# Kernel optimization log

Hardware: AMD Instinct MI355X
Metric: run time of the kernel (lower is better)

The kernel has to match this reference:

```python
import jax, jax.numpy as jnp
import numpy as np

N_NODES = 50000
N_EDGES = 800000
IN_DIM = 128
OUT_DIM = 128
NUM_RELS = 8


def setup_inputs() -> dict:
    key = jax.random.key(0)
    k_feat, k_rel, k_w, k_src, k_dst, k_rt = jax.random.split(key, 6)
    feat = jax.random.normal(k_feat, (N_NODES, IN_DIM), dtype=jnp.float32)
    # xavier_uniform over (in_dim, out_dim) fan
    limit = float(np.sqrt(6.0 / (IN_DIM + OUT_DIM)))
    rel_emb = jax.random.uniform(k_rel, (NUM_RELS, IN_DIM, OUT_DIM), dtype=jnp.float32,
                                 minval=-limit, maxval=limit)
    edge_weight = jax.random.uniform(k_w, (N_EDGES,), dtype=jnp.float32)
    src = jax.random.randint(k_src, (N_EDGES,), 0, N_NODES, dtype=jnp.int32)
    dst = jax.random.randint(k_dst, (N_EDGES,), 0, N_NODES, dtype=jnp.int32)
    rel_type = jax.random.randint(k_rt, (N_EDGES,), 0, NUM_RELS, dtype=jnp.int32)
    return {"feat": feat, "rel_emb": rel_emb, "edge_weight": edge_weight,
            "src": src, "dst": dst, "rel_type": rel_type}


def reference(feat, rel_emb, edge_weight, src, dst, rel_type):
    # src_feat: [E, in] gather of source-node features
    src_feat = feat[src]
    num_rels = rel_emb.shape[0]
    # Equivalent to bmm(src_feat[:,None,:], rel_emb[rel_type]).squeeze(1)
    # but avoids materializing the [E, in, out] per-edge weight tensor:
    # loop over the small fixed relation set with masked accumulation.
    msg = jnp.zeros((src_feat.shape[0], rel_emb.shape[2]), dtype=src_feat.dtype)
    for r in range(num_rels):
        mask = (rel_type == r)[:, None]
        msg = msg + jnp.where(mask, src_feat @ rel_emb[r], jnp.zeros((), dtype=src_feat.dtype))
    msg = msg * edge_weight[:, None]
    # copy_e + sum aggregation onto destination nodes: [N, out]
    return jax.ops.segment_sum(msg, dst, num_segments=feat.shape[0])
```

## Files before the change

### kernel.cpp

```cpp
#include <hip/hip_runtime.h>
#include <stdint.h>

#define N_NODES   50000
#define N_EDGES   800000
#define IN_DIM    128
#define OUT_DIM   128
#define NUM_RELS  8
#define THREADS   256

typedef _Float16 half_t;
typedef _Float16 half2v __attribute__((ext_vector_type(2)));
typedef _Float16 half4v __attribute__((ext_vector_type(4)));
typedef _Float16 half8 __attribute__((ext_vector_type(8)));
typedef float floatx4 __attribute__((ext_vector_type(4)));


#define NBINS3    N_NODES
#define NB3       ((NBINS3 + 1023) / 1024)

#define WS_Y2     0
#define WS_OFF    102400000
#define WS_WT     102600064
#define WS_BASE   102862208
#define WS_WGT    106062208
#define WS_HIST   107662208
#define WS_BSUM   107862208
#define WS_NEED   (size_t)107862464

#define HIST_BLOCKS ((N_EDGES + 511) / 512)
__global__ void prep_hist_kernel(const float* __restrict__ rel_emb, half_t* __restrict__ WT,
                                 const int* __restrict__ dst, int* __restrict__ hist) {
    int b = blockIdx.x;
    if (b < 512) {
        int t = b * 256 + threadIdx.x;
        int r = t >> 14, k = (t >> 7) & 127, n = t & 127;
        WT[(size_t)((r << 7) | n) * 128 + k] = (half_t)rel_emb[t];
    } else {
        int i = (b - 512) * 512 + threadIdx.x;
        int d0 = (i < N_EDGES) ? dst[i] : -1;
        int d1 = (i + 256 < N_EDGES) ? dst[i + 256] : -1;
        if (d0 >= 0) atomicAdd(&hist[d0], 1);
        if (d1 >= 0) atomicAdd(&hist[d1], 1);
    }
}

__global__ void scan1_kernel(const int* __restrict__ hist, int* __restrict__ bsum) {
    __shared__ int sh[256];
    int b = blockIdx.x, t = threadIdx.x;
    int i0 = b * 1024 + t * 4;
    int s = 0;
    #pragma unroll
    for (int j = 0; j < 4; j++) { int idx = i0 + j; if (idx < NBINS3) s += hist[idx]; }
    sh[t] = s; __syncthreads();
    for (int o = 128; o > 0; o >>= 1) { if (t < o) sh[t] += sh[t + o]; __syncthreads(); }
    if (t == 0) bsum[b] = sh[0];
}

__global__ void scan2_kernel(int* __restrict__ bsum, int* __restrict__ off) {
    __shared__ int sh[64];
    int t = threadIdx.x;
    int v = (t < NB3) ? bsum[t] : 0;
    sh[t] = v; __syncthreads();
    for (int o = 1; o < 64; o <<= 1) {
        int x = (t >= o) ? sh[t - o] : 0;
        __syncthreads();
        sh[t] += x;
        __syncthreads();
    }
    if (t < NB3) bsum[t] = sh[t] - v;
    if (t == 0) off[NBINS3] = N_EDGES;
}

__global__ void scan3_kernel(const int* __restrict__ hist, const int* __restrict__ boff,
                             int* __restrict__ off, int* __restrict__ cursors) {
    __shared__ int sh[256];
    int b = blockIdx.x, t = threadIdx.x;
    int i0 = b * 1024 + t * 4;
    int v[4]; int s = 0;
    #pragma unroll
    for (int j = 0; j < 4; j++) { int idx = i0 + j; v[j] = (idx < NBINS3) ? hist[idx] : 0; s += v[j]; }
    sh[t] = s; __syncthreads();
    for (int o = 1; o < 256; o <<= 1) {
        int x = (t >= o) ? sh[t - o] : 0;
        __syncthreads();
        sh[t] += x;
        __syncthreads();
    }
    int run = sh[t] - s + boff[b];
    #pragma unroll
    for (int j = 0; j < 4; j++) {
        int idx = i0 + j;
        if (idx < NBINS3) { off[idx] = run; cursors[idx] = run; }
        run += v[j];
    }
}

template<bool GUARD>
__device__ __forceinline__ void gemm_body(const float* __restrict__ feat,
                                          half_t* __restrict__ Ws,
                                          half_t* __restrict__ y2,
                                          int m0, int n0, int wave, int lane) {
    const int q = lane >> 4, l16 = lane & 15;
    const int wm0 = m0 + wave * 32;

    float4 fr[2][4][2];
    #pragma unroll
    for (int ms = 0; ms < 2; ms++) {
        int node = wm0 + ms * 16 + l16;
        const float* fb = feat + (size_t)node * 128 + q * 8;
        bool ok = !GUARD || node < N_NODES;
        #pragma unroll
        for (int kk = 0; kk < 4; kk++)
            #pragma unroll
            for (int h = 0; h < 2; h++) {
                float4 v = {0.f, 0.f, 0.f, 0.f};
                if (ok) v = *(const float4*)(fb + kk * 32 + h * 4);
                fr[ms][kk][h] = v;
            }
    }
    __syncthreads();

    half8 bf[2][4];
    #pragma unroll
    for (int ms = 0; ms < 2; ms++)
        #pragma unroll
        for (int kk = 0; kk < 4; kk++) {
            half8 hb;
            hb[0] = (half_t)fr[ms][kk][0].x; hb[1] = (half_t)fr[ms][kk][0].y;
            hb[2] = (half_t)fr[ms][kk][0].z; hb[3] = (half_t)fr[ms][kk][0].w;
            hb[4] = (half_t)fr[ms][kk][1].x; hb[5] = (half_t)fr[ms][kk][1].y;
            hb[6] = (half_t)fr[ms][kk][1].z; hb[7] = (half_t)fr[ms][kk][1].w;
            bf[ms][kk] = hb;
        }

    floatx4 acc[8][2];
    #pragma unroll
    for (int nt = 0; nt < 8; nt++)
        #pragma unroll
        for (int ms = 0; ms < 2; ms++) acc[nt][ms] = (floatx4){0.f, 0.f, 0.f, 0.f};

    #pragma unroll
    for (int kk = 0; kk < 4; kk++) {
        #pragma unroll
        for (int nt = 0; nt < 8; nt++) {
            int row = nt * 16 + l16;
            int phys = (kk * 4 + q) ^ (l16 & 7);
            half8 a = *(const half8*)(Ws + row * 128 + phys * 8);
            acc[nt][0] = __builtin_amdgcn_mfma_f32_16x16x32_f16(a, bf[0][kk], acc[nt][0], 0, 0, 0);
            acc[nt][1] = __builtin_amdgcn_mfma_f32_16x16x32_f16(a, bf[1][kk], acc[nt][1], 0, 0, 0);
        }
    }

    __syncthreads();
    #pragma unroll
    for (int nt = 0; nt < 8; nt++)
        #pragma unroll
        for (int ms = 0; ms < 2; ms++) {
            int nl = wave * 32 + ms * 16 + l16;
            int c  = nt * 4 + q;
            int p  = (c + nl) & 31;
            half4v hv;
            hv[0] = (half_t)acc[nt][ms][0]; hv[1] = (half_t)acc[nt][ms][1];
            hv[2] = (half_t)acc[nt][ms][2]; hv[3] = (half_t)acc[nt][ms][3];
            *(half4v*)(Ws + nl * 128 + p * 4) = hv;
        }
    #pragma unroll
    for (int i = 0; i < 8; i++) {
        int nl  = wave * 32 + i * 4 + (lane >> 4);
        int c16 = lane & 15;
        int p0 = (2 * c16 + nl) & 31;
        int p1 = (2 * c16 + 1 + nl) & 31;
        uint2 lo = *(const uint2*)(Ws + nl * 128 + p0 * 4);
        uint2 hi = *(const uint2*)(Ws + nl * 128 + p1 * 4);
        int node = m0 + nl;
        if (!GUARD || node < N_NODES) {
            uint4 v; v.x = lo.x; v.y = lo.y; v.z = hi.x; v.w = hi.y;
            *(uint4*)(y2 + (size_t)node * 1024 + n0 + c16 * 8) = v;
        }
    }
}

#define FUSE_BLOCKS 6256
__global__ __launch_bounds__(THREADS) void fused_kernel(
    const float* __restrict__ feat, const half_t* __restrict__ WT,
    half_t* __restrict__ y2,
    const int* __restrict__ dst, const int* __restrict__ src,
    const int* __restrict__ rel, const float* __restrict__ ew,
    int* __restrict__ cursors, int* __restrict__ base, half_t* __restrict__ wgt) {
    __shared__ half_t Ws[128 * 128];
    const int bid = blockIdx.x;
    const int t = threadIdx.x;

    if (((bid >> 3) & 1) == 0) {
        int work = (bid & 7) * 391 + (bid >> 4);
        int mt = work >> 3, nt8 = work & 7;
        const int m0 = mt * 128, n0 = nt8 * 128;
        const int wave = t >> 6, lane = t & 63;

        for (int i = t; i < 2048; i += THREADS) {
            int row = i >> 4, lc = i & 15;
            int phys = lc ^ (row & 7);
            *(uint4*)&Ws[row * 128 + phys * 8] =
                *(const uint4*)(WT + (size_t)(n0 + row) * 128 + lc * 8);
        }
        if (m0 + 128 <= N_NODES)
            gemm_body<false>(feat, Ws, y2, m0, n0, wave, lane);
        else
            gemm_body<true>(feat, Ws, y2, m0, n0, wave, lane);
    } else {
        int sblock = (bid >> 4) * 8 + (bid & 7);
        if (sblock >= 3125) return;
        int i = sblock * 256 + t;
        int pos = atomicAdd(&cursors[dst[i]], 1);
        base[pos] = src[i] * 1024 + rel[i] * 128;
        wgt[pos] = (half_t)ew[i];
    }
}

__global__ __launch_bounds__(THREADS) void gather_kernel(
    const half_t* __restrict__ y2, const int* __restrict__ base,
    const half_t* __restrict__ wgt, const int* __restrict__ off,
    float* __restrict__ out) {
    int g = blockIdx.x * 4 + (threadIdx.x >> 6);
    int lane = threadIdx.x & 63;
    int beg = off[g], end = off[g + 1];
    const half_t* yb = y2 + lane * 2;
    float ax = 0.f, ay = 0.f, cx = 0.f, cy = 0.f;
    int e = beg;
    for (; e + 8 <= end; e += 8) {
        int b0 = base[e], b1 = base[e + 1], b2 = base[e + 2], b3 = base[e + 3];
        int b4 = base[e + 4], b5 = base[e + 5], b6 = base[e + 6], b7 = base[e + 7];
        half2v v0 = *(const half2v*)(yb + b0);
        half2v v1 = *(const half2v*)(yb + b1);
        half2v v2 = *(const half2v*)(yb + b2);
        half2v v3 = *(const half2v*)(yb + b3);
        half2v v4 = *(const half2v*)(yb + b4);
        half2v v5 = *(const half2v*)(yb + b5);
        half2v v6 = *(const half2v*)(yb + b6);
        half2v v7 = *(const half2v*)(yb + b7);
        float w0 = (float)wgt[e],     w1 = (float)wgt[e + 1];
        float w2 = (float)wgt[e + 2], w3 = (float)wgt[e + 3];
        float w4 = (float)wgt[e + 4], w5 = (float)wgt[e + 5];
        float w6 = (float)wgt[e + 6], w7 = (float)wgt[e + 7];
        ax += w0 * (float)v0[0] + w1 * (float)v1[0];
        ay += w0 * (float)v0[1] + w1 * (float)v1[1];
        cx += w2 * (float)v2[0] + w3 * (float)v3[0];
        cy += w2 * (float)v2[1] + w3 * (float)v3[1];
        ax += w4 * (float)v4[0] + w5 * (float)v5[0];
        ay += w4 * (float)v4[1] + w5 * (float)v5[1];
        cx += w6 * (float)v6[0] + w7 * (float)v7[0];
        cy += w6 * (float)v6[1] + w7 * (float)v7[1];
    }
    for (; e + 2 <= end; e += 2) {
        int b0 = base[e], b1 = base[e + 1];
        float w0 = (float)wgt[e], w1 = (float)wgt[e + 1];
        half2v v0 = *(const half2v*)(yb + b0);
        half2v v1 = *(const half2v*)(yb + b1);
        ax += w0 * (float)v0[0] + w1 * (float)v1[0];
        ay += w0 * (float)v0[1] + w1 * (float)v1[1];
    }
    if (e < end) {
        int b0 = base[e];
        float w0 = (float)wgt[e];
        half2v v0 = *(const half2v*)(yb + b0);
        cx += w0 * (float)v0[0];
        cy += w0 * (float)v0[1];
    }
    float2 o; o.x = ax + cx; o.y = ay + cy;
    *(float2*)(out + (size_t)g * 128 + lane * 2) = o;
}

__global__ void naive_kernel(const float* __restrict__ feat, const float* __restrict__ rel_emb,
                             const float* __restrict__ ew, const int* __restrict__ src,
                             const int* __restrict__ dst, const int* __restrict__ rel,
                             float* __restrict__ out) {
    int wave = (blockIdx.x * blockDim.x + threadIdx.x) >> 6;
    int lane = threadIdx.x & 63;
    if (wave >= N_EDGES) return;
    const float* f = feat + (size_t)src[wave] * IN_DIM;
    const float* W = rel_emb + (size_t)rel[wave] * IN_DIM * OUT_DIM;
    float w = ew[wave];
    float a0 = 0.f, a1 = 0.f;
    for (int k = 0; k < IN_DIM; k++) {
        float fv = f[k];
        a0 += fv * W[k * OUT_DIM + lane];
        a1 += fv * W[k * OUT_DIM + 64 + lane];
    }
    int d = dst[wave];
    atomicAdd(&out[(size_t)d * OUT_DIM + lane], a0 * w);
    atomicAdd(&out[(size_t)d * OUT_DIM + 64 + lane], a1 * w);
}

extern "C" void kernel_launch(void* const* d_in, const int* in_sizes, int n_in,
                              void* d_out, int out_size, void* d_ws, size_t ws_size,
                              hipStream_t stream) {
    const float* feat    = (const float*)d_in[0];
    const float* rel_emb = (const float*)d_in[1];
    const float* ew      = (const float*)d_in[2];
    const int*   src     = (const int*)d_in[3];
    const int*   dst     = (const int*)d_in[4];
    const int*   rel     = (const int*)d_in[5];
    float* out = (float*)d_out;

    if (ws_size >= WS_NEED) {
        char* ws = (char*)d_ws;
        half_t* y2    = (half_t*)(ws + WS_Y2);
        int*    off   = (int*)(ws + WS_OFF);
        half_t* WT    = (half_t*)(ws + WS_WT);
        int*    basep = (int*)(ws + WS_BASE);
        half_t* wgt   = (half_t*)(ws + WS_WGT);
        int*    hist  = (int*)(ws + WS_HIST);
        int*    bsum  = (int*)(ws + WS_BSUM);

        hipMemsetAsync(hist, 0, (size_t)NBINS3 * 4, stream);
        prep_hist_kernel<<<512 + HIST_BLOCKS, THREADS, 0, stream>>>(rel_emb, WT, dst, hist);
        scan1_kernel<<<NB3, 256, 0, stream>>>(hist, bsum);
        scan2_kernel<<<1, 64, 0, stream>>>(bsum, off);
        scan3_kernel<<<NB3, 256, 0, stream>>>(hist, bsum, off, hist);
        fused_kernel<<<FUSE_BLOCKS, THREADS, 0, stream>>>(feat, WT, y2, dst, src, rel, ew,
                                                          hist, basep, wgt);
        gather_kernel<<<N_NODES / 4, THREADS, 0, stream>>>(y2, basep, wgt, off, out);
    } else {
        hipMemsetAsync(d_out, 0, (size_t)out_size * sizeof(float), stream);
        const long long total = (long long)N_EDGES * 64;
        const int blocks = (int)((total + THREADS - 1) / THREADS);
        naive_kernel<<<blocks, THREADS, 0, stream>>>(feat, rel_emb, ew, src, dst, rel, out);
    }
}
```

Measured before the change: 260.7 us.

## Widen gather loads to 16B per lane and batch histogram/scatter edges per thread

The gather kernel now splits each wave into four 16-lane groups. Each group handles a different edge and loads 16-byte half8 vectors instead of 4-byte half2. Partial sums are combined with cross-group shuffles before one lane group writes the output row. The histogram and scatter phases each process four edges per thread with the loads hoisted ahead of the atomics, which increases memory-level parallelism. The cost is more registers, a shuffle reduction per node, and partial-group waste when a node has few edges.

```diff
diff --git a/kernel.cpp b/kernel.cpp
--- a/kernel.cpp
+++ b/kernel.cpp
@@ -27,7 +27,7 @@
 #define WS_BSUM   107862208
 #define WS_NEED   (size_t)107862464
 
-#define HIST_BLOCKS ((N_EDGES + 511) / 512)
+#define HIST_BLOCKS ((N_EDGES + 1023) / 1024)
 __global__ void prep_hist_kernel(const float* __restrict__ rel_emb, half_t* __restrict__ WT,
                                  const int* __restrict__ dst, int* __restrict__ hist) {
     int b = blockIdx.x;
@@ -36,11 +36,16 @@
         int r = t >> 14, k = (t >> 7) & 127, n = t & 127;
         WT[(size_t)((r << 7) | n) * 128 + k] = (half_t)rel_emb[t];
     } else {
-        int i = (b - 512) * 512 + threadIdx.x;
-        int d0 = (i < N_EDGES) ? dst[i] : -1;
-        int d1 = (i + 256 < N_EDGES) ? dst[i + 256] : -1;
-        if (d0 >= 0) atomicAdd(&hist[d0], 1);
-        if (d1 >= 0) atomicAdd(&hist[d1], 1);
+        int i0 = (b - 512) * 1024 + threadIdx.x;
+        int d[4];
+        #pragma unroll
+        for (int j = 0; j < 4; j++) {
+            int i = i0 + j * 256;
+            d[j] = (i < N_EDGES) ? dst[i] : -1;
+        }
+        #pragma unroll
+        for (int j = 0; j < 4; j++)
+            if (d[j] >= 0) atomicAdd(&hist[d[j]], 1);
     }
 }
 
@@ -209,11 +214,24 @@
             gemm_body<true>(feat, Ws, y2, m0, n0, wave, lane);
     } else {
         int sblock = (bid >> 4) * 8 + (bid & 7);
-        if (sblock >= 3125) return;
-        int i = sblock * 256 + t;
-        int pos = atomicAdd(&cursors[dst[i]], 1);
-        base[pos] = src[i] * 1024 + rel[i] * 128;
-        wgt[pos] = (half_t)ew[i];
+        if (sblock >= HIST_BLOCKS) return;
+        int i0 = sblock * 1024 + t;
+        int d[4], s[4], r[4]; float w[4];
+        #pragma unroll
+        for (int j = 0; j < 4; j++) {
+            int i = i0 + j * 256;
+            d[j] = (i < N_EDGES) ? dst[i] : -1;
+            s[j] = 0; r[j] = 0; w[j] = 0.f;
+            if (d[j] >= 0) { s[j] = src[i]; r[j] = rel[i]; w[j] = ew[i]; }
+        }
+        #pragma unroll
+        for (int j = 0; j < 4; j++) {
+            if (d[j] >= 0) {
+                int pos = atomicAdd(&cursors[d[j]], 1);
+                base[pos] = s[j] * 1024 + r[j] * 128;
+                wgt[pos] = (half_t)w[j];
+            }
+        }
     }
 }
 
@@ -223,51 +241,47 @@
     float* __restrict__ out) {
     int g = blockIdx.x * 4 + (threadIdx.x >> 6);
     int lane = threadIdx.x & 63;
+    int q = lane >> 4, l16 = lane & 15;
     int beg = off[g], end = off[g + 1];
-    const half_t* yb = y2 + lane * 2;
-    float ax = 0.f, ay = 0.f, cx = 0.f, cy = 0.f;
+    const half_t* yb = y2 + l16 * 8;
+    float a0[8], a1[8];
+    #pragma unroll
+    for (int j = 0; j < 8; j++) { a0[j] = 0.f; a1[j] = 0.f; }
     int e = beg;
     for (; e + 8 <= end; e += 8) {
-        int b0 = base[e], b1 = base[e + 1], b2 = base[e + 2], b3 = base[e + 3];
-        int b4 = base[e + 4], b5 = base[e + 5], b6 = base[e + 6], b7 = base[e + 7];
-        half2v v0 = *(const half2v*)(yb + b0);
-        half2v v1 = *(const half2v*)(yb + b1);
-        half2v v2 = *(const half2v*)(yb + b2);
-        half2v v3 = *(const half2v*)(yb + b3);
-        half2v v4 = *(const half2v*)(yb + b4);
-        half2v v5 = *(const half2v*)(yb + b5);
-        half2v v6 = *(const half2v*)(yb + b6);
-        half2v v7 = *(const half2v*)(yb + b7);
-        float w0 = (float)wgt[e],     w1 = (float)wgt[e + 1];
-        float w2 = (float)wgt[e + 2], w3 = (float)wgt[e + 3];
-        float w4 = (float)wgt[e + 4], w5 = (float)wgt[e + 5];
-        float w6 = (float)wgt[e + 6], w7 = (float)wgt[e + 7];
-        ax += w0 * (float)v0[0] + w1 * (float)v1[0];
-        ay += w0 * (float)v0[1] + w1 * (float)v1[1];
-        cx += w2 * (float)v2[0] + w3 * (float)v3[0];
-        cy += w2 * (float)v2[1] + w3 * (float)v3[1];
-        ax += w4 * (float)v4[0] + w5 * (float)v5[0];
-        ay += w4 * (float)v4[1] + w5 * (float)v5[1];
-        cx += w6 * (float)v6[0] + w7 * (float)v7[0];
-        cy += w6 * (float)v6[1] + w7 * (float)v7[1];
-    }
-    for (; e + 2 <= end; e += 2) {
-        int b0 = base[e], b1 = base[e + 1];
-        float w0 = (float)wgt[e], w1 = (float)wgt[e + 1];
-        half2v v0 = *(const half2v*)(yb + b0);
-        half2v v1 = *(const half2v*)(yb + b1);
-        ax += w0 * (float)v0[0] + w1 * (float)v1[0];
-        ay += w0 * (float)v0[1] + w1 * (float)v1[1];
-    }
-    if (e < end) {
-        int b0 = base[e];
-        float w0 = (float)wgt[e];
-        half2v v0 = *(const half2v*)(yb + b0);
-        cx += w0 * (float)v0[0];
-        cy += w0 * (float)v0[1];
-    }
-    float2 o; o.x = ax + cx; o.y = ay + cy;
-    *(float2*)(out + (size_t)g * 128 + lane * 2) = o;
+        int e0 = e + q, e1 = e + 4 + q;
+        int b0 = base[e0], b1 = base[e1];
+        float w0 = (float)wgt[e0], w1 = (float)wgt[e1];
+        half8 v0 = *(const half8*)(yb + b0);
+        half8 v1 = *(const half8*)(yb + b1);
+        #pragma unroll
+        for (int j = 0; j < 8; j++) a0[j] += w0 * (float)v0[j];
+        #pragma unroll
+        for (int j = 0; j < 8; j++) a1[j] += w1 * (float)v1[j];
+    }
+    for (; e < end; e += 4) {
+        int ee = e + q;
+        int b0 = 0; float w0 = 0.f;
+        if (ee < end) { b0 = base[ee]; w0 = (float)wgt[ee]; }
+        half8 v0 = *(const half8*)(yb + b0);
+        #pragma unroll
+        for (int j = 0; j < 8; j++) a0[j] += w0 * (float)v0[j];
+    }
+    #pragma unroll
+    for (int j = 0; j < 8; j++) {
+        float s = a0[j] + a1[j];
+        s += __shfl_xor(s, 16);
+        s += __shfl_xor(s, 32);
+        a0[j] = s;
+    }
+    if (q == 0) {
+        float4 o0, o1;
+        o0.x = a0[0]; o0.y = a0[1]; o0.z = a0[2]; o0.w = a0[3];
+        o1.x = a0[4]; o1.y = a0[5]; o1.z = a0[6]; o1.w = a0[7];
+        float* ob = out + (size_t)g * 128 + l16 * 8;
+        *(float4*)ob = o0;
+        *(float4*)(ob + 4) = o1;
+    }
 }
 
 __global__ void naive_kernel(const float* __restrict__ feat, const float* __restrict__ rel_emb,
```

Result: no change. 257.6 us (-1.2%).

## Aggregate source features per relation before GEMM, using linked-list edge buckets

Applied to the files above, without the earlier changes.

The pipeline now aggregates weighted source features per destination node and per relation first, then runs one GEMM with K=1024 against the stacked relation weights, instead of transforming every node for all relations and gathering afterwards. The histogram plus three scan kernels are replaced by an atomicExch linked list built from dst. Launches drop from six kernels to three, and the y2 scatter buffer is replaced by an fp16 h buffer of the same size. The cost is a serial pointer-chasing walk per node with dependent loads, a per-edge branch on relation type, and edge order within each node that depends on atomic ordering.

```diff
diff --git a/kernel.cpp b/kernel.cpp
--- a/kernel.cpp
+++ b/kernel.cpp
@@ -10,264 +10,143 @@
 
 typedef _Float16 half_t;
 typedef _Float16 half2v __attribute__((ext_vector_type(2)));
-typedef _Float16 half4v __attribute__((ext_vector_type(4)));
 typedef _Float16 half8 __attribute__((ext_vector_type(8)));
 typedef float floatx4 __attribute__((ext_vector_type(4)));
 
 
-#define NBINS3    N_NODES
-#define NB3       ((NBINS3 + 1023) / 1024)
-
-#define WS_Y2     0
-#define WS_OFF    102400000
-#define WS_WT     102600064
-#define WS_BASE   102862208
-#define WS_WGT    106062208
-#define WS_HIST   107662208
-#define WS_BSUM   107862208
-#define WS_NEED   (size_t)107862464
-
-#define HIST_BLOCKS ((N_EDGES + 511) / 512)
-__global__ void prep_hist_kernel(const float* __restrict__ rel_emb, half_t* __restrict__ WT,
-                                 const int* __restrict__ dst, int* __restrict__ hist) {
+#define WS_H      0
+#define WS_WFT    102400000
+#define WS_HEAD   102662144
+#define WS_NEXT   102862144
+#define WS_NEED3  (size_t)106062144
+
+#define LIST_BLOCKS (N_EDGES / 256)
+
+__global__ void prep_kernel(const float* __restrict__ rel_emb, half_t* __restrict__ WfT,
+                            const int* __restrict__ dst, int* __restrict__ head,
+                            int* __restrict__ next) {
     int b = blockIdx.x;
     if (b < 512) {
         int t = b * 256 + threadIdx.x;
         int r = t >> 14, k = (t >> 7) & 127, n = t & 127;
-        WT[(size_t)((r << 7) | n) * 128 + k] = (half_t)rel_emb[t];
+        WfT[(size_t)n * 1024 + r * 128 + k] = (half_t)rel_emb[t];
     } else {
-        int i = (b - 512) * 512 + threadIdx.x;
-        int d0 = (i < N_EDGES) ? dst[i] : -1;
-        int d1 = (i + 256 < N_EDGES) ? dst[i + 256] : -1;
-        if (d0 >= 0) atomicAdd(&hist[d0], 1);
-        if (d1 >= 0) atomicAdd(&hist[d1], 1);
-    }
-}
-
-__global__ void scan1_kernel(const int* __restrict__ hist, int* __restrict__ bsum) {
-    __shared__ int sh[256];
-    int b = blockIdx.x, t = threadIdx.x;
-    int i0 = b * 1024 + t * 4;
-    int s = 0;
+        int i = (b - 512) * 256 + threadIdx.x;
+        next[i] = atomicExch(&head[dst[i]], i);
+    }
+}
+
+__global__ __launch_bounds__(THREADS) void agg_kernel(
+    const float* __restrict__ feat, const float* __restrict__ ew,
+    const int* __restrict__ src, const int* __restrict__ rel,
+    const int* __restrict__ head, const int* __restrict__ next,
+    half_t* __restrict__ h) {
+    int g = blockIdx.x * 4 + (threadIdx.x >> 6);
+    int lane = threadIdx.x & 63;
+
+    float a0x = 0.f, a0y = 0.f, a1x = 0.f, a1y = 0.f;
+    float a2x = 0.f, a2y = 0.f, a3x = 0.f, a3y = 0.f;
+    float a4x = 0.f, a4y = 0.f, a5x = 0.f, a5y = 0.f;
+    float a6x = 0.f, a6y = 0.f, a7x = 0.f, a7y = 0.f;
+
+    int e = head[g];
+    while (e >= 0) {
+        int nx  = next[e];
+        int sr  = src[e];
+        int re  = rel[e];
+        float w = ew[e];
+        float2 f = *(const float2*)(feat + (size_t)sr * 128 + lane * 2);
+        float wx = w * f.x, wy = w * f.y;
+        switch (re) {
+            case 0: a0x += wx; a0y += wy; break;
+            case 1: a1x += wx; a1y += wy; break;
+            case 2: a2x += wx; a2y += wy; break;
+            case 3: a3x += wx; a3y += wy; break;
+            case 4: a4x += wx; a4y += wy; break;
+            case 5: a5x += wx; a5y += wy; break;
+            case 6: a6x += wx; a6y += wy; break;
+            default: a7x += wx; a7y += wy; break;
+        }
+        e = nx;
+    }
+
+    half_t* hb = h + (size_t)g * 1024 + lane * 2;
+    *(half2v*)(hb + 0 * 128) = (half2v){(half_t)a0x, (half_t)a0y};
+    *(half2v*)(hb + 1 * 128) = (half2v){(half_t)a1x, (half_t)a1y};
+    *(half2v*)(hb + 2 * 128) = (half2v){(half_t)a2x, (half_t)a2y};
+    *(half2v*)(hb + 3 * 128) = (half2v){(half_t)a3x, (half_t)a3y};
+    *(half2v*)(hb + 4 * 128) = (half2v){(half_t)a4x, (half_t)a4y};
+    *(half2v*)(hb + 5 * 128) = (half2v){(half_t)a5x, (half_t)a5y};
+    *(half2v*)(hb + 6 * 128) = (half2v){(half_t)a6x, (half_t)a6y};
+    *(half2v*)(hb + 7 * 128) = (half2v){(half_t)a7x, (half_t)a7y};
+}
+
+template<bool GUARD>
+__device__ __forceinline__ void gemm2_body(const half_t* __restrict__ h,
+                                           const half_t* __restrict__ WfT,
+                                           half_t* __restrict__ Ws,
+                                           float* __restrict__ out,
+                                           int m0, int wave, int lane, int t) {
+    const int q = lane >> 4, l16 = lane & 15;
+    const int d = m0 + wave * 16 + l16;
+    const bool ok = !GUARD || d < N_NODES;
+    const half_t* hb = h + (size_t)d * 1024;
+
+    floatx4 acc[8];
     #pragma unroll
-    for (int j = 0; j < 4; j++) { int idx = i0 + j; if (idx < NBINS3) s += hist[idx]; }
-    sh[t] = s; __syncthreads();
-    for (int o = 128; o > 0; o >>= 1) { if (t < o) sh[t] += sh[t + o]; __syncthreads(); }
-    if (t == 0) bsum[b] = sh[0];
-}
-
-__global__ void scan2_kernel(int* __restrict__ bsum, int* __restrict__ off) {
-    __shared__ int sh[64];
-    int t = threadIdx.x;
-    int v = (t < NB3) ? bsum[t] : 0;
-    sh[t] = v; __syncthreads();
-    for (int o = 1; o < 64; o <<= 1) {
-        int x = (t >= o) ? sh[t - o] : 0;
-        __syncthreads();
-        sh[t] += x;
-        __syncthreads();
-    }
-    if (t < NB3) bsum[t] = sh[t] - v;
-    if (t == 0) off[NBINS3] = N_EDGES;
-}
-
-__global__ void scan3_kernel(const int* __restrict__ hist, const int* __restrict__ boff,
-                             int* __restrict__ off, int* __restrict__ cursors) {
-    __shared__ int sh[256];
-    int b = blockIdx.x, t = threadIdx.x;
-    int i0 = b * 1024 + t * 4;
-    int v[4]; int s = 0;
+    for (int nt = 0; nt < 8; nt++) acc[nt] = (floatx4){0.f, 0.f, 0.f, 0.f};
+
     #pragma unroll
-    for (int j = 0; j < 4; j++) { int idx = i0 + j; v[j] = (idx < NBINS3) ? hist[idx] : 0; s += v[j]; }
-    sh[t] = s; __syncthreads();
-    for (int o = 1; o < 256; o <<= 1) {
-        int x = (t >= o) ? sh[t - o] : 0;
-        __syncthreads();
-        sh[t] += x;
-        __syncthreads();
-    }
-    int run = sh[t] - s + boff[b];
-    #pragma unroll
-    for (int j = 0; j < 4; j++) {
-        int idx = i0 + j;
-        if (idx < NBINS3) { off[idx] = run; cursors[idx] = run; }
-        run += v[j];
-    }
-}
-
-template<bool GUARD>
-__device__ __forceinline__ void gemm_body(const float* __restrict__ feat,
-                                          half_t* __restrict__ Ws,
-                                          half_t* __restrict__ y2,
-                                          int m0, int n0, int wave, int lane) {
-    const int q = lane >> 4, l16 = lane & 15;
-    const int wm0 = m0 + wave * 32;
-
-    float4 fr[2][4][2];
-    #pragma unroll
-    for (int ms = 0; ms < 2; ms++) {
-        int node = wm0 + ms * 16 + l16;
-        const float* fb = feat + (size_t)node * 128 + q * 8;
-        bool ok = !GUARD || node < N_NODES;
-        #pragma unroll
-        for (int kk = 0; kk < 4; kk++)
-            #pragma unroll
-            for (int h = 0; h < 2; h++) {
-                float4 v = {0.f, 0.f, 0.f, 0.f};
-                if (ok) v = *(const float4*)(fb + kk * 32 + h * 4);
-                fr[ms][kk][h] = v;
-            }
-    }
-    __syncthreads();
-
-    half8 bf[2][4];
-    #pragma unroll
-    for (int ms = 0; ms < 2; ms++)
+    for (int kc = 0; kc < 8; kc++) {
+        half8 bf[4];
         #pragma unroll
         for (int kk = 0; kk < 4; kk++) {
-            half8 hb;
-            hb[0] = (half_t)fr[ms][kk][0].x; hb[1] = (half_t)fr[ms][kk][0].y;
-            hb[2] = (half_t)fr[ms][kk][0].z; hb[3] = (half_t)fr[ms][kk][0].w;
-            hb[4] = (half_t)fr[ms][kk][1].x; hb[5] = (half_t)fr[ms][kk][1].y;
-            hb[6] = (half_t)fr[ms][kk][1].z; hb[7] = (half_t)fr[ms][kk][1].w;
-            bf[ms][kk] = hb;
-        }
-
-    floatx4 acc[8][2];
-    #pragma unroll
-    for (int nt = 0; nt < 8; nt++)
-        #pragma unroll
-        for (int ms = 0; ms < 2; ms++) acc[nt][ms] = (floatx4){0.f, 0.f, 0.f, 0.f};
-
-    #pragma unroll
-    for (int kk = 0; kk < 4; kk++) {
-        #pragma unroll
-        for (int nt = 0; nt < 8; nt++) {
-            int row = nt * 16 + l16;
-            int phys = (kk * 4 + q) ^ (l16 & 7);
-            half8 a = *(const half8*)(Ws + row * 128 + phys * 8);
-            acc[nt][0] = __builtin_amdgcn_mfma_f32_16x16x32_f16(a, bf[0][kk], acc[nt][0], 0, 0, 0);
-            acc[nt][1] = __builtin_amdgcn_mfma_f32_16x16x32_f16(a, bf[1][kk], acc[nt][1], 0, 0, 0);
-        }
-    }
-
-    __syncthreads();
-    #pragma unroll
-    for (int nt = 0; nt < 8; nt++)
-        #pragma unroll
-        for (int ms = 0; ms < 2; ms++) {
-            int nl = wave * 32 + ms * 16 + l16;
-            int c  = nt * 4 + q;
-            int p  = (c + nl) & 31;
-            half4v hv;
-            hv[0] = (half_t)acc[nt][ms][0]; hv[1] = (half_t)acc[nt][ms][1];
-            hv[2] = (half_t)acc[nt][ms][2]; hv[3] = (half_t)acc[nt][ms][3];
-            *(half4v*)(Ws + nl * 128 + p * 4) = hv;
-        }
-    #pragma unroll
-    for (int i = 0; i < 8; i++) {
-        int nl  = wave * 32 + i * 4 + (lane >> 4);
-        int c16 = lane & 15;
-        int p0 = (2 * c16 + nl) & 31;
-        int p1 = (2 * c16 + 1 + nl) & 31;
-        uint2 lo = *(const uint2*)(Ws + nl * 128 + p0 * 4);
-        uint2 hi = *(const uint2*)(Ws + nl * 128 + p1 * 4);
-        int node = m0 + nl;
-        if (!GUARD || node < N_NODES) {
-            uint4 v; v.x = lo.x; v.y = lo.y; v.z = hi.x; v.w = hi.y;
-            *(uint4*)(y2 + (size_t)node * 1024 + n0 + c16 * 8) = v;
-        }
-    }
-}
-
-#define FUSE_BLOCKS 6256
-__global__ __launch_bounds__(THREADS) void fused_kernel(
-    const float* __restrict__ feat, const half_t* __restrict__ WT,
-    half_t* __restrict__ y2,
-    const int* __restrict__ dst, const int* __restrict__ src,
-    const int* __restrict__ rel, const float* __restrict__ ew,
-    int* __restrict__ cursors, int* __restrict__ base, half_t* __restrict__ wgt) {
-    __shared__ half_t Ws[128 * 128];
-    const int bid = blockIdx.x;
-    const int t = threadIdx.x;
-
-    if (((bid >> 3) & 1) == 0) {
-        int work = (bid & 7) * 391 + (bid >> 4);
-        int mt = work >> 3, nt8 = work & 7;
-        const int m0 = mt * 128, n0 = nt8 * 128;
-        const int wave = t >> 6, lane = t & 63;
-
+            uint4 v = {0u, 0u, 0u, 0u};
+            if (ok) v = *(const uint4*)(hb + kc * 128 + kk * 32 + q * 8);
+            bf[kk] = *(half8*)&v;
+        }
+        __syncthreads();
         for (int i = t; i < 2048; i += THREADS) {
             int row = i >> 4, lc = i & 15;
             int phys = lc ^ (row & 7);
             *(uint4*)&Ws[row * 128 + phys * 8] =
-                *(const uint4*)(WT + (size_t)(n0 + row) * 128 + lc * 8);
-        }
-        if (m0 + 128 <= N_NODES)
-            gemm_body<false>(feat, Ws, y2, m0, n0, wave, lane);
-        else
-            gemm_body<true>(feat, Ws, y2, m0, n0, wave, lane);
-    } else {
-        int sblock = (bid >> 4) * 8 + (bid & 7);
-        if (sblock >= 3125) return;
-        int i = sblock * 256 + t;
-        int pos = atomicAdd(&cursors[dst[i]], 1);
-        base[pos] = src[i] * 1024 + rel[i] * 128;
-        wgt[pos] = (half_t)ew[i];
-    }
-}
-
-__global__ __launch_bounds__(THREADS) void gather_kernel(
-    const half_t* __restrict__ y2, const int* __restrict__ base,
-    const half_t* __restrict__ wgt, const int* __restrict__ off,
+                *(const uint4*)(WfT + (size_t)row * 1024 + kc * 128 + lc * 8);
+        }
+        __syncthreads();
+        #pragma unroll
+        for (int kk = 0; kk < 4; kk++)
+            #pragma unroll
+            for (int nt = 0; nt < 8; nt++) {
+                int row = nt * 16 + l16;
+                int phys = (kk * 4 + q) ^ (l16 & 7);
+                half8 a = *(const half8*)(Ws + row * 128 + phys * 8);
+                acc[nt] = __builtin_amdgcn_mfma_f32_16x16x32_f16(a, bf[kk], acc[nt], 0, 0, 0);
+            }
+    }
+
+    if (ok) {
+        float* ob = out + (size_t)d * 128;
+        #pragma unroll
+        for (int nt = 0; nt < 8; nt++) {
+            float4 v;
+            v.x = acc[nt][0]; v.y = acc[nt][1]; v.z = acc[nt][2]; v.w = acc[nt][3];
+            *(float4*)(ob + nt * 16 + q * 4) = v;
+        }
+    }
+}
+
+#define G2_BLOCKS ((N_NODES + 63) / 64)
+__global__ __launch_bounds__(THREADS) void gemm2_kernel(
+    const half_t* __restrict__ h, const half_t* __restrict__ WfT,
     float* __restrict__ out) {
-    int g = blockIdx.x * 4 + (threadIdx.x >> 6);
-    int lane = threadIdx.x & 63;
-    int beg = off[g], end = off[g + 1];
-    const half_t* yb = y2 + lane * 2;
-    float ax = 0.f, ay = 0.f, cx = 0.f, cy = 0.f;
-    int e = beg;
-    for (; e + 8 <= end; e += 8) {
-        int b0 = base[e], b1 = base[e + 1], b2 = base[e + 2], b3 = base[e + 3];
-        int b4 = base[e + 4], b5 = base[e + 5], b6 = base[e + 6], b7 = base[e + 7];
-        half2v v0 = *(const half2v*)(yb + b0);
-        half2v v1 = *(const half2v*)(yb + b1);
-        half2v v2 = *(const half2v*)(yb + b2);
-        half2v v3 = *(const half2v*)(yb + b3);
-        half2v v4 = *(const half2v*)(yb + b4);
-        half2v v5 = *(const half2v*)(yb + b5);
-        half2v v6 = *(const half2v*)(yb + b6);
-        half2v v7 = *(const half2v*)(yb + b7);
-        float w0 = (float)wgt[e],     w1 = (float)wgt[e + 1];
-        float w2 = (float)wgt[e + 2], w3 = (float)wgt[e + 3];
-        float w4 = (float)wgt[e + 4], w5 = (float)wgt[e + 5];
-        float w6 = (float)wgt[e + 6], w7 = (float)wgt[e + 7];
-        ax += w0 * (float)v0[0] + w1 * (float)v1[0];
-        ay += w0 * (float)v0[1] + w1 * (float)v1[1];
-        cx += w2 * (float)v2[0] + w3 * (float)v3[0];
-        cy += w2 * (float)v2[1] + w3 * (float)v3[1];
-        ax += w4 * (float)v4[0] + w5 * (float)v5[0];
-        ay += w4 * (float)v4[1] + w5 * (float)v5[1];
-        cx += w6 * (float)v6[0] + w7 * (float)v7[0];
-        cy += w6 * (float)v6[1] + w7 * (float)v7[1];
-    }
-    for (; e + 2 <= end; e += 2) {
-        int b0 = base[e], b1 = base[e + 1];
-        float w0 = (float)wgt[e], w1 = (float)wgt[e + 1];
-        half2v v0 = *(const half2v*)(yb + b0);
-        half2v v1 = *(const half2v*)(yb + b1);
-        ax += w0 * (float)v0[0] + w1 * (float)v1[0];
-        ay += w0 * (float)v0[1] + w1 * (float)v1[1];
-    }
-    if (e < end) {
-        int b0 = base[e];
-        float w0 = (float)wgt[e];
-        half2v v0 = *(const half2v*)(yb + b0);
-        cx += w0 * (float)v0[0];
-        cy += w0 * (float)v0[1];
-    }
-    float2 o; o.x = ax + cx; o.y = ay + cy;
-    *(float2*)(out + (size_t)g * 128 + lane * 2) = o;
+    __shared__ half_t Ws[128 * 128];
+    const int m0 = blockIdx.x * 64;
+    const int t = threadIdx.x;
+    const int wave = t >> 6, lane = t & 63;
+    if (m0 + 64 <= N_NODES)
+        gemm2_body<false>(h, WfT, Ws, out, m0, wave, lane, t);
+    else
+        gemm2_body<true>(h, WfT, Ws, out, m0, wave, lane, t);
 }
 
 __global__ void naive_kernel(const float* __restrict__ feat, const float* __restrict__ rel_emb,
@@ -302,24 +181,17 @@
     const int*   rel     = (const int*)d_in[5];
     float* out = (float*)d_out;
 
-    if (ws_size >= WS_NEED) {
+    if (ws_size >= WS_NEED3) {
         char* ws = (char*)d_ws;
-        half_t* y2    = (half_t*)(ws + WS_Y2);
-        int*    off   = (int*)(ws + WS_OFF);
-        half_t* WT    = (half_t*)(ws + WS_WT);
-        int*    basep = (int*)(ws + WS_BASE);
-        half_t* wgt   = (half_t*)(ws + WS_WGT);
-        int*    hist  = (int*)(ws + WS_HIST);
-        int*    bsum  = (int*)(ws + WS_BSUM);
-
-        hipMemsetAsync(hist, 0, (size_t)NBINS3 * 4, stream);
-        prep_hist_kernel<<<512 + HIST_BLOCKS, THREADS, 0, stream>>>(rel_emb, WT, dst, hist);
-        scan1_kernel<<<NB3, 256, 0, stream>>>(hist, bsum);
-        scan2_kernel<<<1, 64, 0, stream>>>(bsum, off);
-        scan3_kernel<<<NB3, 256, 0, stream>>>(hist, bsum, off, hist);
-        fused_kernel<<<FUSE_BLOCKS, THREADS, 0, stream>>>(feat, WT, y2, dst, src, rel, ew,
-                                                          hist, basep, wgt);
-        gather_kernel<<<N_NODES / 4, THREADS, 0, stream>>>(y2, basep, wgt, off, out);
+        half_t* h    = (half_t*)(ws + WS_H);
+        half_t* WfT  = (half_t*)(ws + WS_WFT);
+        int*    head = (int*)(ws + WS_HEAD);
+        int*    next = (int*)(ws + WS_NEXT);
+
+        hipMemsetAsync(head, 0xFF, (size_t)N_NODES * 4, stream);
+        prep_kernel<<<512 + LIST_BLOCKS, THREADS, 0, stream>>>(rel_emb, WfT, dst, head, next);
+        agg_kernel<<<N_NODES / 4, THREADS, 0, stream>>>(feat, ew, src, rel, head, next, h);
+        gemm2_kernel<<<G2_BLOCKS, THREADS, 0, stream>>>(h, WfT, out);
     } else {
         hipMemsetAsync(d_out, 0, (size_t)out_size * sizeof(float), stream);
         const long long total = (long long)N_EDGES * 64;
```

New measurement: 346.3 us. 1.33x slower.
